# Kernel optimization log

Hardware: AMD Instinct MI355X
Metric: run time of the kernel (lower is better)

## Reference

```python
import jax, jax.numpy as jnp
import numpy as np

B, C_IN, C_OUT, H, W = 32, 64, 128, 56, 56


def setup_inputs() -> dict:
    key = jax.random.key(0)
    k1, k2, k3 = jax.random.split(key, 3)
    x = jax.random.normal(k1, (B, C_IN, H, W), dtype=jnp.float32)
    # Original build(): kernel ~ N(0,1) in spatial domain, then fft2d; the
    # real/imag parts of the spectrum are the learned variables.
    kernel = jax.random.normal(k2, (C_OUT, C_IN, H, W), dtype=jnp.float32)
    kernel_fft = jnp.fft.fft2(kernel.astype(jnp.complex64))
    kernel_real = jnp.real(kernel_fft).astype(jnp.float32)
    kernel_imag = jnp.imag(kernel_fft).astype(jnp.float32)
    bias = jnp.zeros((C_OUT,), dtype=jnp.float32)
    return {"x": x, "kernel_real": kernel_real, "kernel_imag": kernel_imag, "bias": bias}


def reference(x, kernel_real, kernel_imag, bias):
    # FFT-based convolution, vectorized over batch (original used a per-batch
    # Python loop + concat; math is identical).
    x_fft = jnp.fft.fft2(x.astype(jnp.complex64))              # [B, Cin, H, W]
    kernel_freq = jax.lax.complex(kernel_real, kernel_imag)    # [Cout, Cin, H, W]
    # elementwise complex multiply + reduce over input channels
    y_fft = jnp.einsum('oihw,bihw->bohw', kernel_freq, x_fft)  # [B, Cout, H, W]
    y = jnp.real(jnp.fft.ifft2(y_fft))                         # [B, Cout, H, W]
    return y + bias[None, :, None, None]
```

## Files before the change

kernel.cpp:

```cpp
#include <hip/hip_runtime.h>


#define HH 56
#define NF 3136
#define KH 29
#define NFH 1624
constexpr int B = 32, CIN = 64, COUT = 128;
constexpr float PI2 = 6.283185307179586f;

typedef unsigned short u16;
typedef __attribute__((ext_vector_type(8))) short s8v;
typedef __attribute__((ext_vector_type(4))) float f4v;
typedef __attribute__((ext_vector_type(4))) int i4v;

#define MFMA(a, b, c) __builtin_amdgcn_mfma_f32_16x16x32_bf16(a, b, c, 0, 0, 0)

__device__ __host__ inline short f2bf(float f) {
    unsigned u = __builtin_bit_cast(unsigned, f);
    u += 0x7fffu + ((u >> 16) & 1u);
    return (short)(u >> 16);
}

__device__ inline s8v negbf(s8v a) {
    i4v t = __builtin_bit_cast(i4v, a);
    t ^= (int)0x80008000u;
    return __builtin_bit_cast(s8v, t);
}

__global__ __launch_bounds__(256) void ksetup(short* __restrict__ cpool) {
    int i = blockIdx.x * 256 + threadIdx.x;
    if (i < 4608) {
        int m = i / 72, n = i % 72;
        float c = 0.f, s = 0.f;
        if (m < 56 && n < 56) {
            float ang = PI2 * (float)((m * n) % 56) / 56.f;
            c = cosf(ang); s = sinf(ang);
        }
        cpool[i]        = f2bf(c);
        cpool[4608 + i] = f2bf(s);
        cpool[9216 + i] = f2bf(-s);
    } else if (i < 7168) {
        int j = i - 4608;
        int h = j / 40, kh = j % 40;
        float c = 0.f, s = 0.f;
        if (h < 56 && kh < 29) {
            float w = (kh == 0 || kh == 28) ? 1.f : 2.f;
            float ang = PI2 * (float)((h * kh) % 56) / 56.f;
            float sc = w * (1.f / 3136.f);
            c = sc * cosf(ang);
            s = -sc * sinf(ang);
        }
        cpool[13824 + j] = f2bf(c);
        cpool[16384 + j] = f2bf(s);
    }
}

__global__ __launch_bounds__(256) void kprep(const float* __restrict__ Kr,
                                             const float* __restrict__ Ki,
                                             u16* __restrict__ Kbr,
                                             u16* __restrict__ Kbi) {
    __shared__ u16 Lr[64 * 57], Li[64 * 57];
    const int tid = threadIdx.x;
    const int oi0 = blockIdx.x * 64;
    const int f0  = blockIdx.y * 56;
    for (int idx = tid; idx < 3584; idx += 256) {
        int row = idx / 56, f = idx % 56;
        size_t g = (size_t)(oi0 + row) * NF + f0 + f;
        Lr[row * 57 + f] = (u16)f2bf(Kr[g]);
        Li[row * 57 + f] = (u16)f2bf(Ki[g]);
    }
    __syncthreads();
    for (int idx = tid; idx < 3584; idx += 256) {
        int f = idx >> 6, j = idx & 63;
        size_t o = (size_t)(f0 + f) * 8192 + oi0 + j;
        Kbr[o] = Lr[j * 57 + f];
        Kbi[o] = Li[j * 57 + f];
    }
}

__global__ __launch_bounds__(256) void kfwd(const float* __restrict__ x,
                                            const short* __restrict__ cpool,
                                            ushort2* __restrict__ Xb) {
    __shared__ __align__(16) short Cw[4608], Sw[4608], SwN[4608];
    __shared__ __align__(16) short xs[4608];
    __shared__ __align__(16) short T1r[4608], T1i[4608];
    const int tid = threadIdx.x;
    {
        const int4* src = (const int4*)cpool;
        for (int i = tid; i < 576; i += 256) {
            ((int4*)Cw)[i]  = src[i];
            ((int4*)Sw)[i]  = src[576 + i];
            ((int4*)SwN)[i] = src[1152 + i];
        }
    }
    for (int i = tid; i < 2304; i += 256) ((int*)xs)[i] = 0;
    __syncthreads();
    const float* xp = x + (size_t)blockIdx.x * NF;
    for (int i = tid; i < NF; i += 256) {
        int h = i / 56, w = i % 56;
        xs[h * 72 + w] = f2bf(xp[i]);
    }
    __syncthreads();

    const int lane = tid & 63;
    const int nt = tid >> 6;
    const int q = lane >> 4, l15 = lane & 15;

    f4v aR[4] = {}, aI[4] = {};
    for (int ks = 0; ks < 2; ++ks) {
        const int bo = (nt * 16 + l15) * 72 + ks * 32 + q * 8;
        s8v bC = *(const s8v*)&Cw[bo];
        s8v bS = *(const s8v*)&SwN[bo];
        for (int mt = 0; mt < 4; ++mt) {
            s8v a = *(const s8v*)&xs[(mt * 16 + l15) * 72 + ks * 32 + q * 8];
            aR[mt] = MFMA(a, bC, aR[mt]);
            aI[mt] = MFMA(a, bS, aI[mt]);
        }
    }
    for (int mt = 0; mt < 4; ++mt)
        for (int r = 0; r < 4; ++r) {
            int o = (nt * 16 + l15) * 72 + mt * 16 + q * 4 + r;
            T1r[o] = f2bf(aR[mt][r]);
            T1i[o] = f2bf(aI[mt][r]);
        }
    __syncthreads();

    f4v xr[2] = {}, xi2[2] = {};
    for (int ks = 0; ks < 2; ++ks) {
        const int bo = (nt * 16 + l15) * 72 + ks * 32 + q * 8;
        s8v br = *(const s8v*)&T1r[bo];
        s8v bi = *(const s8v*)&T1i[bo];
        for (int mt = 0; mt < 2; ++mt) {
            const int ao = (mt * 16 + l15) * 72 + ks * 32 + q * 8;
            s8v aC  = *(const s8v*)&Cw[ao];
            s8v aS  = *(const s8v*)&Sw[ao];
            s8v aSN = *(const s8v*)&SwN[ao];
            xr[mt]  = MFMA(aC, br, xr[mt]);
            xr[mt]  = MFMA(aS, bi, xr[mt]);
            xi2[mt] = MFMA(aC, bi, xi2[mt]);
            xi2[mt] = MFMA(aSN, br, xi2[mt]);
        }
    }
    ushort2* op = Xb + (size_t)blockIdx.x * NFH;
    const int kw = nt * 16 + l15;
    if (kw < 56) {
        for (int mt = 0; mt < 2; ++mt)
            for (int r = 0; r < 4; ++r) {
                int kh = mt * 16 + q * 4 + r;
                if (kh < 29)
                    op[kh * 56 + kw] = make_ushort2((u16)f2bf(xr[mt][r]),
                                                    (u16)f2bf(xi2[mt][r]));
            }
    }
}

__global__ __launch_bounds__(512) void kmix(const ushort2* __restrict__ Xb,
                                            const u16* __restrict__ Kbr,
                                            const u16* __restrict__ Kbi,
                                            ushort2* __restrict__ Yb) {
    __shared__ __align__(16) u16 Xr[8 * 2304], Xi[8 * 2304];
    const int tid = threadIdx.x;
    const int f0 = blockIdx.x * 8;

    for (int rr = 0; rr < 4; ++rr) {
        int row = rr * 512 + tid;
        const uint4* src = (const uint4*)(Xb + (size_t)row * NFH + f0);
        uint4 v0 = src[0], v1 = src[1];
        int base = (row >> 6) * 72 + (row & 63);
        unsigned uu[8] = {v0.x, v0.y, v0.z, v0.w, v1.x, v1.y, v1.z, v1.w};
        #pragma unroll
        for (int ff = 0; ff < 8; ++ff) {
            Xr[ff * 2304 + base] = (u16)uu[ff];
            Xi[ff * 2304 + base] = (u16)(uu[ff] >> 16);
        }
    }
    __syncthreads();

    const int lane = tid & 63;
    const int wv = tid >> 6;
    const int q = lane >> 4, l15 = lane & 15;

    unsigned pk[2][4][8];

    #pragma unroll
    for (int ff = 0; ff < 8; ++ff) {
        const int f = f0 + ff;
        const size_t kb = (size_t)f * 8192 + (size_t)(wv * 16 + l15) * 64 + q * 8;
        s8v bkr0 = *(const s8v*)&Kbr[kb];
        s8v bkr1 = *(const s8v*)&Kbr[kb + 32];
        s8v bki0 = *(const s8v*)&Kbi[kb];
        s8v bki1 = *(const s8v*)&Kbi[kb + 32];

        f4v yr[2] = {}, yi[2] = {};
        #pragma unroll
        for (int mt = 0; mt < 2; ++mt) {
            const int ao = ff * 2304 + (mt * 16 + l15) * 72 + q * 8;
            s8v axr0 = *(const s8v*)&Xr[ao];
            s8v axr1 = *(const s8v*)&Xr[ao + 32];
            s8v axi0 = *(const s8v*)&Xi[ao];
            s8v axi1 = *(const s8v*)&Xi[ao + 32];
            s8v axn0 = negbf(axi0), axn1 = negbf(axi1);
            yr[mt] = MFMA(axr0, bkr0, yr[mt]);
            yr[mt] = MFMA(axn0, bki0, yr[mt]);
            yr[mt] = MFMA(axr1, bkr1, yr[mt]);
            yr[mt] = MFMA(axn1, bki1, yr[mt]);
            yi[mt] = MFMA(axr0, bki0, yi[mt]);
            yi[mt] = MFMA(axi0, bkr0, yi[mt]);
            yi[mt] = MFMA(axr1, bki1, yi[mt]);
            yi[mt] = MFMA(axi1, bkr1, yi[mt]);
        }
        #pragma unroll
        for (int mt = 0; mt < 2; ++mt)
            #pragma unroll
            for (int r = 0; r < 4; ++r)
                pk[mt][r][ff] = (unsigned)(u16)f2bf(yr[mt][r]) |
                                ((unsigned)(u16)f2bf(yi[mt][r]) << 16);
    }

    const int o = wv * 16 + l15;
    #pragma unroll
    for (int mt = 0; mt < 2; ++mt)
        #pragma unroll
        for (int r = 0; r < 4; ++r) {
            const int b = mt * 16 + q * 4 + r;
            uint4* dst = (uint4*)(Yb + (size_t)(b * COUT + o) * NFH + f0);
            dst[0] = make_uint4(pk[mt][r][0], pk[mt][r][1],
                                pk[mt][r][2], pk[mt][r][3]);
            dst[1] = make_uint4(pk[mt][r][4], pk[mt][r][5],
                                pk[mt][r][6], pk[mt][r][7]);
        }
}

__global__ __launch_bounds__(256) void kinv(const ushort2* __restrict__ Yf,
                                            const short* __restrict__ cpool,
                                            const float* __restrict__ bias,
                                            float* __restrict__ out) {
    __shared__ __align__(16) short Cw[4608], Sw[4608], SwN[4608];
    __shared__ __align__(16) short A2C[2560], A2S[2560];
    __shared__ __align__(16) short Yr[2304], Yi[2304];
    __shared__ __align__(16) short ZTr[2560], ZTi[2560];
    const int tid = threadIdx.x;
    {
        const int4* src = (const int4*)cpool;
        for (int i = tid; i < 576; i += 256) {
            ((int4*)Cw)[i]  = src[i];
            ((int4*)Sw)[i]  = src[576 + i];
            ((int4*)SwN)[i] = src[1152 + i];
        }
        for (int i = tid; i < 320; i += 256) {
            ((int4*)A2C)[i] = src[1728 + i];
            ((int4*)A2S)[i] = src[2048 + i];
        }
    }
    for (int i = tid; i < 1152; i += 256) { ((int*)Yr)[i] = 0; ((int*)Yi)[i] = 0; }
    __syncthreads();
    const ushort2* yp = Yf + (size_t)blockIdx.x * NFH;
    for (int f = tid; f < NFH; f += 256) {
        int kh = f / 56, kw = f % 56;
        ushort2 v = yp[f];
        Yr[kh * 72 + kw] = (short)v.x;
        Yi[kh * 72 + kw] = (short)v.y;
    }
    __syncthreads();

    const int lane = tid & 63;
    const int nt = tid >> 6;
    const int q = lane >> 4, l15 = lane & 15;

    f4v zr[2] = {}, zi[2] = {};
    for (int ks = 0; ks < 2; ++ks) {
        const int bo = (nt * 16 + l15) * 72 + ks * 32 + q * 8;
        s8v bC  = *(const s8v*)&Cw[bo];
        s8v bS  = *(const s8v*)&Sw[bo];
        s8v bSN = *(const s8v*)&SwN[bo];
        for (int mt = 0; mt < 2; ++mt) {
            const int ao = (mt * 16 + l15) * 72 + ks * 32 + q * 8;
            s8v ar = *(const s8v*)&Yr[ao];
            s8v ai = *(const s8v*)&Yi[ao];
            zr[mt] = MFMA(ar, bC, zr[mt]);
            zr[mt] = MFMA(ai, bSN, zr[mt]);
            zi[mt] = MFMA(ar, bS, zi[mt]);
            zi[mt] = MFMA(ai, bC, zi[mt]);
        }
    }
    for (int mt = 0; mt < 2; ++mt)
        for (int r = 0; r < 4; ++r) {
            int o = (nt * 16 + l15) * 40 + mt * 16 + q * 4 + r;
            ZTr[o] = f2bf(zr[mt][r]);
            ZTi[o] = f2bf(zi[mt][r]);
        }
    __syncthreads();

    f4v yv[4] = {};
    {
        const int bo = (nt * 16 + l15) * 40 + q * 8;
        s8v br = *(const s8v*)&ZTr[bo];
        s8v bi = *(const s8v*)&ZTi[bo];
        for (int mt = 0; mt < 4; ++mt) {
            const int ao = (mt * 16 + l15) * 40 + q * 8;
            s8v ac  = *(const s8v*)&A2C[ao];
            s8v as_ = *(const s8v*)&A2S[ao];
            yv[mt] = MFMA(ac, br, yv[mt]);
            yv[mt] = MFMA(as_, bi, yv[mt]);
        }
    }
    const float bv = bias[blockIdx.x & (COUT - 1)];
    float* opx = out + (size_t)blockIdx.x * NF;
    const int w = nt * 16 + l15;
    if (w < 56) {
        for (int mt = 0; mt < 4; ++mt)
            for (int r = 0; r < 4; ++r) {
                int h = mt * 16 + q * 4 + r;
                if (h < 56) opx[h * 56 + w] = yv[mt][r] + bv;
            }
    }
}

extern "C" void kernel_launch(void* const* d_in, const int* in_sizes, int n_in,
                              void* d_out, int out_size, void* d_ws, size_t ws_size,
                              hipStream_t stream) {
    const float* x    = (const float*)d_in[0];
    const float* Kr   = (const float*)d_in[1];
    const float* Ki   = (const float*)d_in[2];
    const float* bias = (const float*)d_in[3];

    short*   cpool = (short*)d_ws;
    ushort2* Xb  = (ushort2*)((char*)d_ws + 40960);
    ushort2* Yb  = (ushort2*)((char*)d_ws + 40960 + 13307904);
    u16*     Kbr = (u16*)((char*)d_ws + 40960 + 13307904 + 26615808);
    u16*     Kbi = Kbr + (size_t)13307904;

    hipLaunchKernelGGL(ksetup, dim3(28), dim3(256), 0, stream, cpool);
    hipLaunchKernelGGL(kprep, dim3(128, 29), dim3(256), 0, stream, Kr, Ki, Kbr, Kbi);
    hipLaunchKernelGGL(kfwd, dim3(B * CIN), dim3(256), 0, stream, x, cpool, Xb);
    hipLaunchKernelGGL(kmix, dim3(NFH / 8), dim3(512), 0, stream, Xb, Kbr, Kbi, Yb);
    hipLaunchKernelGGL(kinv, dim3(B * COUT), dim3(256), 0, stream,
                       Yb, cpool, bias, (float*)d_out);
}
```

Baseline: 343.7 us.

## Process two images per block, vectorize loads/stores, compute negated sine on the fly

The forward and inverse DFT kernels now handle two images per 512-thread block, so each block loads the twiddle tables once for two images instead of once per image. The precomputed negated-sine table is dropped and replaced by a sign-bit flip in registers, which reduces shared memory per image. Global loads and LDS stores in kprep, kfwd and kinv are widened to float4/uint2/uint4 with packed bf16 pairs, replacing the scalar element stores. The costs are larger blocks with more shared memory each, which may lower occupancy, and extra XOR instructions for the negation.

After: 305.4 us. -11.2%, faster.

```diff
diff --git a/kernel.cpp b/kernel.cpp
--- a/kernel.cpp
+++ b/kernel.cpp
@@ -19,6 +19,10 @@
     unsigned u = __builtin_bit_cast(unsigned, f);
     u += 0x7fffu + ((u >> 16) & 1u);
     return (short)(u >> 16);
+}
+
+__device__ inline unsigned pk2(float a, float b) {
+    return (unsigned)(u16)f2bf(a) | ((unsigned)(u16)f2bf(b) << 16);
 }
 
 __device__ inline s8v negbf(s8v a) {
@@ -38,7 +42,6 @@
         }
         cpool[i]        = f2bf(c);
         cpool[4608 + i] = f2bf(s);
-        cpool[9216 + i] = f2bf(-s);
     } else if (i < 7168) {
         int j = i - 4608;
         int h = j / 40, kh = j % 40;
@@ -59,89 +62,101 @@
                                              const float* __restrict__ Ki,
                                              u16* __restrict__ Kbr,
                                              u16* __restrict__ Kbi) {
-    __shared__ u16 Lr[64 * 57], Li[64 * 57];
+    __shared__ __align__(8) u16 Lr[64 * 60], Li[64 * 60];
     const int tid = threadIdx.x;
     const int oi0 = blockIdx.x * 64;
     const int f0  = blockIdx.y * 56;
-    for (int idx = tid; idx < 3584; idx += 256) {
-        int row = idx / 56, f = idx % 56;
-        size_t g = (size_t)(oi0 + row) * NF + f0 + f;
-        Lr[row * 57 + f] = (u16)f2bf(Kr[g]);
-        Li[row * 57 + f] = (u16)f2bf(Ki[g]);
-    }
-    __syncthreads();
-    for (int idx = tid; idx < 3584; idx += 256) {
-        int f = idx >> 6, j = idx & 63;
-        size_t o = (size_t)(f0 + f) * 8192 + oi0 + j;
-        Kbr[o] = Lr[j * 57 + f];
-        Kbi[o] = Li[j * 57 + f];
-    }
-}
-
-__global__ __launch_bounds__(256) void kfwd(const float* __restrict__ x,
+    for (int c = tid; c < 896; c += 256) {
+        int row = c / 14, c4 = (c % 14) * 4;
+        size_t g = (size_t)(oi0 + row) * NF + f0 + c4;
+        float4 vr = *(const float4*)&Kr[g];
+        float4 vi = *(const float4*)&Ki[g];
+        *(uint2*)&Lr[row * 60 + c4] = make_uint2(pk2(vr.x, vr.y), pk2(vr.z, vr.w));
+        *(uint2*)&Li[row * 60 + c4] = make_uint2(pk2(vi.x, vi.y), pk2(vi.z, vi.w));
+    }
+    __syncthreads();
+    for (int idx = tid; idx < 896; idx += 256) {
+        int c = idx & 15, f = idx >> 4;
+        int j0 = c * 4;
+        unsigned r01 = (unsigned)Lr[j0 * 60 + f]       | ((unsigned)Lr[(j0 + 1) * 60 + f] << 16);
+        unsigned r23 = (unsigned)Lr[(j0 + 2) * 60 + f] | ((unsigned)Lr[(j0 + 3) * 60 + f] << 16);
+        unsigned i01 = (unsigned)Li[j0 * 60 + f]       | ((unsigned)Li[(j0 + 1) * 60 + f] << 16);
+        unsigned i23 = (unsigned)Li[(j0 + 2) * 60 + f] | ((unsigned)Li[(j0 + 3) * 60 + f] << 16);
+        size_t o = (size_t)(f0 + f) * 8192 + oi0 + j0;
+        *(uint2*)&Kbr[o] = make_uint2(r01, r23);
+        *(uint2*)&Kbi[o] = make_uint2(i01, i23);
+    }
+}
+
+__global__ __launch_bounds__(512) void kfwd(const float* __restrict__ x,
                                             const short* __restrict__ cpool,
                                             ushort2* __restrict__ Xb) {
-    __shared__ __align__(16) short Cw[4608], Sw[4608], SwN[4608];
-    __shared__ __align__(16) short xs[4608];
-    __shared__ __align__(16) short T1r[4608], T1i[4608];
+    __shared__ __align__(16) short Cw[4608], Sw[4608];
+    __shared__ __align__(16) short xs[2][4608];
+    __shared__ __align__(16) short T1r[2][4608], T1i[2][4608];
     const int tid = threadIdx.x;
     {
         const int4* src = (const int4*)cpool;
-        for (int i = tid; i < 576; i += 256) {
-            ((int4*)Cw)[i]  = src[i];
-            ((int4*)Sw)[i]  = src[576 + i];
-            ((int4*)SwN)[i] = src[1152 + i];
-        }
-    }
-    for (int i = tid; i < 2304; i += 256) ((int*)xs)[i] = 0;
-    __syncthreads();
-    const float* xp = x + (size_t)blockIdx.x * NF;
-    for (int i = tid; i < NF; i += 256) {
-        int h = i / 56, w = i % 56;
-        xs[h * 72 + w] = f2bf(xp[i]);
+        for (int i = tid; i < 576; i += 512) {
+            ((int4*)Cw)[i] = src[i];
+            ((int4*)Sw)[i] = src[576 + i];
+        }
+    }
+    for (int i = tid; i < 4608; i += 512) ((int*)xs)[i] = 0;
+    __syncthreads();
+    const int half = tid >> 8, tid2 = tid & 255;
+    const float* xp = x + (size_t)(blockIdx.x * 2 + half) * NF;
+    short* xsh = xs[half];
+    for (int c = tid2; c < 784; c += 256) {
+        int r = c / 14, c4 = (c % 14) * 4;
+        float4 v = *(const float4*)&xp[r * 56 + c4];
+        *(uint2*)&xsh[r * 72 + c4] = make_uint2(pk2(v.x, v.y), pk2(v.z, v.w));
     }
     __syncthreads();
 
     const int lane = tid & 63;
-    const int nt = tid >> 6;
+    const int wv = tid >> 6;
+    const int hw = wv >> 2;
+    const int nt = wv & 3;
     const int q = lane >> 4, l15 = lane & 15;
 
     f4v aR[4] = {}, aI[4] = {};
     for (int ks = 0; ks < 2; ++ks) {
         const int bo = (nt * 16 + l15) * 72 + ks * 32 + q * 8;
-        s8v bC = *(const s8v*)&Cw[bo];
-        s8v bS = *(const s8v*)&SwN[bo];
+        s8v bC  = *(const s8v*)&Cw[bo];
+        s8v bSN = negbf(*(const s8v*)&Sw[bo]);
         for (int mt = 0; mt < 4; ++mt) {
-            s8v a = *(const s8v*)&xs[(mt * 16 + l15) * 72 + ks * 32 + q * 8];
+            s8v a = *(const s8v*)&xs[hw][(mt * 16 + l15) * 72 + ks * 32 + q * 8];
             aR[mt] = MFMA(a, bC, aR[mt]);
-            aI[mt] = MFMA(a, bS, aI[mt]);
-        }
-    }
-    for (int mt = 0; mt < 4; ++mt)
-        for (int r = 0; r < 4; ++r) {
-            int o = (nt * 16 + l15) * 72 + mt * 16 + q * 4 + r;
-            T1r[o] = f2bf(aR[mt][r]);
-            T1i[o] = f2bf(aI[mt][r]);
-        }
+            aI[mt] = MFMA(a, bSN, aI[mt]);
+        }
+    }
+    for (int mt = 0; mt < 4; ++mt) {
+        int o = (nt * 16 + l15) * 72 + mt * 16 + q * 4;
+        *(uint2*)&T1r[hw][o] = make_uint2(pk2(aR[mt][0], aR[mt][1]),
+                                          pk2(aR[mt][2], aR[mt][3]));
+        *(uint2*)&T1i[hw][o] = make_uint2(pk2(aI[mt][0], aI[mt][1]),
+                                          pk2(aI[mt][2], aI[mt][3]));
+    }
     __syncthreads();
 
     f4v xr[2] = {}, xi2[2] = {};
     for (int ks = 0; ks < 2; ++ks) {
         const int bo = (nt * 16 + l15) * 72 + ks * 32 + q * 8;
-        s8v br = *(const s8v*)&T1r[bo];
-        s8v bi = *(const s8v*)&T1i[bo];
+        s8v br = *(const s8v*)&T1r[hw][bo];
+        s8v bi = *(const s8v*)&T1i[hw][bo];
         for (int mt = 0; mt < 2; ++mt) {
             const int ao = (mt * 16 + l15) * 72 + ks * 32 + q * 8;
             s8v aC  = *(const s8v*)&Cw[ao];
             s8v aS  = *(const s8v*)&Sw[ao];
-            s8v aSN = *(const s8v*)&SwN[ao];
+            s8v aSN = negbf(aS);
             xr[mt]  = MFMA(aC, br, xr[mt]);
             xr[mt]  = MFMA(aS, bi, xr[mt]);
             xi2[mt] = MFMA(aC, bi, xi2[mt]);
             xi2[mt] = MFMA(aSN, br, xi2[mt]);
         }
     }
-    ushort2* op = Xb + (size_t)blockIdx.x * NFH;
+    ushort2* op = Xb + (size_t)(blockIdx.x * 2 + hw) * NFH;
     const int kw = nt * 16 + l15;
     if (kw < 56) {
         for (int mt = 0; mt < 2; ++mt)
@@ -231,71 +246,76 @@
         }
 }
 
-__global__ __launch_bounds__(256) void kinv(const ushort2* __restrict__ Yf,
+__global__ __launch_bounds__(512) void kinv(const ushort2* __restrict__ Yf,
                                             const short* __restrict__ cpool,
                                             const float* __restrict__ bias,
                                             float* __restrict__ out) {
-    __shared__ __align__(16) short Cw[4608], Sw[4608], SwN[4608];
+    __shared__ __align__(16) short Cw[4608], Sw[4608];
     __shared__ __align__(16) short A2C[2560], A2S[2560];
-    __shared__ __align__(16) short Yr[2304], Yi[2304];
-    __shared__ __align__(16) short ZTr[2560], ZTi[2560];
+    __shared__ __align__(16) short Yr[2][2304], Yi[2][2304];
+    __shared__ __align__(16) short ZTr[2][2560], ZTi[2][2560];
     const int tid = threadIdx.x;
     {
         const int4* src = (const int4*)cpool;
-        for (int i = tid; i < 576; i += 256) {
-            ((int4*)Cw)[i]  = src[i];
-            ((int4*)Sw)[i]  = src[576 + i];
-            ((int4*)SwN)[i] = src[1152 + i];
-        }
-        for (int i = tid; i < 320; i += 256) {
+        for (int i = tid; i < 576; i += 512) {
+            ((int4*)Cw)[i] = src[i];
+            ((int4*)Sw)[i] = src[576 + i];
+        }
+        for (int i = tid; i < 320; i += 512) {
             ((int4*)A2C)[i] = src[1728 + i];
             ((int4*)A2S)[i] = src[2048 + i];
         }
     }
-    for (int i = tid; i < 1152; i += 256) { ((int*)Yr)[i] = 0; ((int*)Yi)[i] = 0; }
-    __syncthreads();
-    const ushort2* yp = Yf + (size_t)blockIdx.x * NFH;
-    for (int f = tid; f < NFH; f += 256) {
-        int kh = f / 56, kw = f % 56;
-        ushort2 v = yp[f];
-        Yr[kh * 72 + kw] = (short)v.x;
-        Yi[kh * 72 + kw] = (short)v.y;
+    for (int i = tid; i < 2304; i += 512) { ((int*)Yr)[i] = 0; ((int*)Yi)[i] = 0; }
+    __syncthreads();
+    const int half = tid >> 8, tid2 = tid & 255;
+    const ushort2* yp = Yf + (size_t)(blockIdx.x * 2 + half) * NFH;
+    for (int c = tid2; c < 406; c += 256) {
+        uint4 v = *(const uint4*)&yp[c * 4];
+        int f = c * 4, kh = f / 56, kwb = f % 56;
+        int o = kh * 72 + kwb;
+        *(uint2*)&Yr[half][o] = make_uint2((v.x & 0xffffu) | (v.y << 16),
+                                           (v.z & 0xffffu) | (v.w << 16));
+        *(uint2*)&Yi[half][o] = make_uint2((v.x >> 16) | (v.y & 0xffff0000u),
+                                           (v.z >> 16) | (v.w & 0xffff0000u));
     }
     __syncthreads();
 
     const int lane = tid & 63;
-    const int nt = tid >> 6;
+    const int wv = tid >> 6;
+    const int hw = wv >> 2, nt = wv & 3;
     const int q = lane >> 4, l15 = lane & 15;
 
     f4v zr[2] = {}, zi[2] = {};
     for (int ks = 0; ks < 2; ++ks) {
         const int bo = (nt * 16 + l15) * 72 + ks * 32 + q * 8;
-        s8v bC  = *(const s8v*)&Cw[bo];
-        s8v bS  = *(const s8v*)&Sw[bo];
-        s8v bSN = *(const s8v*)&SwN[bo];
+        s8v bC = *(const s8v*)&Cw[bo];
+        s8v bS = *(const s8v*)&Sw[bo];
         for (int mt = 0; mt < 2; ++mt) {
             const int ao = (mt * 16 + l15) * 72 + ks * 32 + q * 8;
-            s8v ar = *(const s8v*)&Yr[ao];
-            s8v ai = *(const s8v*)&Yi[ao];
+            s8v ar  = *(const s8v*)&Yr[hw][ao];
+            s8v ai  = *(const s8v*)&Yi[hw][ao];
+            s8v ain = negbf(ai);
             zr[mt] = MFMA(ar, bC, zr[mt]);
-            zr[mt] = MFMA(ai, bSN, zr[mt]);
+            zr[mt] = MFMA(ain, bS, zr[mt]);
             zi[mt] = MFMA(ar, bS, zi[mt]);
             zi[mt] = MFMA(ai, bC, zi[mt]);
         }
     }
-    for (int mt = 0; mt < 2; ++mt)
-        for (int r = 0; r < 4; ++r) {
-            int o = (nt * 16 + l15) * 40 + mt * 16 + q * 4 + r;
-            ZTr[o] = f2bf(zr[mt][r]);
-            ZTi[o] = f2bf(zi[mt][r]);
-        }
+    for (int mt = 0; mt < 2; ++mt) {
+        int o = (nt * 16 + l15) * 40 + mt * 16 + q * 4;
+        *(uint2*)&ZTr[hw][o] = make_uint2(pk2(zr[mt][0], zr[mt][1]),
+                                          pk2(zr[mt][2], zr[mt][3]));
+        *(uint2*)&ZTi[hw][o] = make_uint2(pk2(zi[mt][0], zi[mt][1]),
+                                          pk2(zi[mt][2], zi[mt][3]));
+    }
     __syncthreads();
 
     f4v yv[4] = {};
     {
         const int bo = (nt * 16 + l15) * 40 + q * 8;
-        s8v br = *(const s8v*)&ZTr[bo];
-        s8v bi = *(const s8v*)&ZTi[bo];
+        s8v br = *(const s8v*)&ZTr[hw][bo];
+        s8v bi = *(const s8v*)&ZTi[hw][bo];
         for (int mt = 0; mt < 4; ++mt) {
             const int ao = (mt * 16 + l15) * 40 + q * 8;
             s8v ac  = *(const s8v*)&A2C[ao];
@@ -304,8 +324,9 @@
             yv[mt] = MFMA(as_, bi, yv[mt]);
         }
     }
-    const float bv = bias[blockIdx.x & (COUT - 1)];
-    float* opx = out + (size_t)blockIdx.x * NF;
+    const int img = blockIdx.x * 2 + hw;
+    const float bv = bias[img & (COUT - 1)];
+    float* opx = out + (size_t)img * NF;
     const int w = nt * 16 + l15;
     if (w < 56) {
         for (int mt = 0; mt < 4; ++mt)
@@ -332,8 +353,8 @@
 
     hipLaunchKernelGGL(ksetup, dim3(28), dim3(256), 0, stream, cpool);
     hipLaunchKernelGGL(kprep, dim3(128, 29), dim3(256), 0, stream, Kr, Ki, Kbr, Kbi);
-    hipLaunchKernelGGL(kfwd, dim3(B * CIN), dim3(256), 0, stream, x, cpool, Xb);
+    hipLaunchKernelGGL(kfwd, dim3(B * CIN / 2), dim3(512), 0, stream, x, cpool, Xb);
     hipLaunchKernelGGL(kmix, dim3(NFH / 8), dim3(512), 0, stream, Xb, Kbr, Kbi, Yb);
-    hipLaunchKernelGGL(kinv, dim3(B * COUT), dim3(256), 0, stream,
+    hipLaunchKernelGGL(kinv, dim3(B * COUT / 2), dim3(512), 0, stream,
                        Yb, cpool, bias, (float*)d_out);
 }
```
